# Performance work log

Measured on AMD Instinct MI355X. Metric: run time of the kernel, lower is better.

Reference implementation:

```python
import jax, jax.numpy as jnp
import numpy as np

N_NODES, N_EDGES, DIM, N_LAYERS, N_GRAPHS, N_CLASSES = 50000, 640000, 128, 5, 512, 128


def setup_inputs() -> dict:
    key = jax.random.key(0)
    ks = jax.random.split(key, 10)
    x = jnp.zeros((N_NODES,), dtype=jnp.int32)  # Embedding(1, D) -> all indices 0
    edge_index = jax.random.randint(ks[0], (2, N_EDGES), 0, N_NODES, dtype=jnp.int32)
    edge_attr = jax.random.normal(ks[1], (N_EDGES, DIM), dtype=jnp.float32)
    batch = jnp.sort(jax.random.randint(ks[2], (N_NODES,), 0, N_GRAPHS, dtype=jnp.int32))
    s = 1.0 / np.sqrt(DIM)
    node_emb = jax.random.normal(ks[3], (1, DIM), dtype=jnp.float32)
    Ws = jax.random.normal(ks[4], (N_LAYERS, DIM, DIM), dtype=jnp.float32) * s
    bs = jnp.zeros((N_LAYERS, DIM), dtype=jnp.float32)
    Wes = jax.random.normal(ks[5], (N_LAYERS, DIM, DIM), dtype=jnp.float32) * s
    Wp = jax.random.normal(ks[6], (DIM, N_CLASSES), dtype=jnp.float32) * s
    bp = jnp.zeros((N_CLASSES,), dtype=jnp.float32)
    return {"x": x, "edge_index": edge_index, "edge_attr": edge_attr, "batch": batch,
            "node_emb": node_emb, "Ws": Ws, "bs": bs, "Wes": Wes, "Wp": Wp, "bp": bp}


def reference(x, edge_index, edge_attr, batch, node_emb, Ws, bs, Wes, Wp, bp):
    src, dst = edge_index[0], edge_index[1]
    h = node_emb[x]  # [N, D] embedding lookup (vocab=1)
    n = h.shape[0]
    e = src.shape[0]
    deg = jax.ops.segment_sum(jnp.ones((e,), h.dtype), dst, num_segments=n)
    deg = jnp.maximum(deg, 1.0)[:, None]  # mean aggregation denominator
    for l in range(N_LAYERS):
        hw = h @ Ws[l] + bs[l]                       # [N, D]
        msg = hw[src] + edge_attr @ Wes[l]           # [E, D] gather + edge transform
        agg = jax.ops.segment_sum(msg, dst, num_segments=n) / deg  # scatter-mean
        h = agg + hw                                 # root connection
        if l < N_LAYERS - 1:
            h = jax.nn.relu(h)                       # relu on all but last layer
        # dropout is identity in eval mode
    g = N_GRAPHS
    cnt = jnp.maximum(jax.ops.segment_sum(jnp.ones((n,), h.dtype), batch, num_segments=g), 1.0)
    pooled = jax.ops.segment_sum(h, batch, num_segments=g) / cnt[:, None]  # global_mean_pool
    return pooled @ Wp + bp  # [G, num_clases]
```

## Files before the change

### kernel.cpp

```cpp
#include <hip/hip_runtime.h>

#define N_NODES   50000
#define N_EDGES   640000
#define DIM       128
#define N_LAYERS  5
#define N_GRAPHS  512
#define N_CLASSES 128
#define NB_SCAN   196

typedef __attribute__((ext_vector_type(8))) short short8;
typedef __attribute__((ext_vector_type(4))) float floatx4;

__device__ inline float bfhi(unsigned u) { return __uint_as_float(u & 0xffff0000u); }
__device__ inline float bflo(unsigned u) { return __uint_as_float(u << 16); }
__device__ inline unsigned f2bf(float f) {
  unsigned x = __float_as_uint(f);
  return (x + 0x7fffu + ((x >> 16) & 1u)) >> 16;
}

__global__ void k_zero(int* __restrict__ deg, int* __restrict__ fill,
                       float* __restrict__ pool, float* __restrict__ cnt) {
  int i = blockIdx.x * 256 + threadIdx.x;
  if (i < N_NODES) { deg[i] = 0; fill[i] = 0; }
  if (i < N_GRAPHS * DIM) pool[i] = 0.f;
  if (i < N_GRAPHS) cnt[i] = 0.f;
}

__global__ void k_deg(const int* __restrict__ dst, int* __restrict__ deg) {
  int e = blockIdx.x * 256 + threadIdx.x;
  if (e < N_EDGES) atomicAdd(&deg[dst[e]], 1);
}

__global__ void k_scan1(const int* __restrict__ deg, int* __restrict__ bsum) {
  __shared__ int s[256];
  int t = threadIdx.x, i = blockIdx.x * 256 + t;
  s[t] = (i < N_NODES) ? deg[i] : 0;
  __syncthreads();
  for (int o = 128; o > 0; o >>= 1) {
    if (t < o) s[t] += s[t + o];
    __syncthreads();
  }
  if (t == 0) bsum[blockIdx.x] = s[0];
}

__global__ void k_scan2(int* __restrict__ bsum) {
  __shared__ int s[256];
  int t = threadIdx.x;
  s[t] = (t < NB_SCAN) ? bsum[t] : 0;
  __syncthreads();
  for (int o = 1; o < 256; o <<= 1) {
    int add = (t >= o) ? s[t - o] : 0;
    __syncthreads();
    s[t] += add;
    __syncthreads();
  }
  int ex = (t == 0) ? 0 : s[t - 1];
  if (t < NB_SCAN) bsum[t] = ex;
}

__global__ void k_scan3(const int* __restrict__ deg, const int* __restrict__ bsum,
                        int* __restrict__ row_ptr) {
  __shared__ int s[256];
  int t = threadIdx.x, i = blockIdx.x * 256 + t;
  s[t] = (i < N_NODES) ? deg[i] : 0;
  __syncthreads();
  for (int o = 1; o < 256; o <<= 1) {
    int add = (t >= o) ? s[t - o] : 0;
    __syncthreads();
    s[t] += add;
    __syncthreads();
  }
  int ex = bsum[blockIdx.x] + ((t == 0) ? 0 : s[t - 1]);
  if (i < N_NODES) row_ptr[i] = ex;
  if (blockIdx.x == 0 && t == 0) row_ptr[N_NODES] = N_EDGES;
}

__global__ void k_fill(const int* __restrict__ src, const int* __restrict__ dst,
                       const int* __restrict__ row_ptr, int* __restrict__ fill,
                       int* __restrict__ col_src, int* __restrict__ col_eid) {
  int e = blockIdx.x * 256 + threadIdx.x;
  if (e < N_EDGES) {
    int d = dst[e];
    int pos = row_ptr[d] + atomicAdd(&fill[d], 1);
    col_src[pos] = src[e];
    col_eid[pos] = e;
  }
}

__global__ void k_wconv(const float* __restrict__ Ws, const float* __restrict__ Wes,
                        unsigned short* __restrict__ Wt_s, unsigned short* __restrict__ Wt_e) {
  int idx = blockIdx.x * 256 + threadIdx.x;
  int which = idx / (N_LAYERS * DIM * DIM);
  int rem = idx - which * (N_LAYERS * DIM * DIM);
  int l = rem >> 14;
  int c = (rem >> 7) & 127;
  int k = rem & 127;
  const float* W = which ? Wes : Ws;
  unsigned short* O = which ? Wt_e : Wt_s;
  float v = W[((size_t)l * DIM + k) * DIM + c];
  O[((size_t)l * DIM + c) * DIM + k] = (unsigned short)f2bf(v);
}

__global__ void k_ean_init(const int* __restrict__ row_ptr, const int* __restrict__ col_eid,
                           const float* __restrict__ edge_attr, const int* __restrict__ x,
                           const float* __restrict__ node_emb,
                           unsigned short* __restrict__ ean, float* __restrict__ rdeg,
                           unsigned short* __restrict__ h) {
  int sub = threadIdx.x >> 5;
  int lane = threadIdx.x & 31;
  int i = blockIdx.x * 8 + sub;
  if (i >= N_NODES) return;
  int b = row_ptr[i], e = row_ptr[i + 1];
  float4 acc = make_float4(0.f, 0.f, 0.f, 0.f);
  for (int p = b; p < e; p++) {
    int eid = col_eid[p];
    float4 v = ((const float4*)(edge_attr + (size_t)eid * DIM))[lane];
    acc.x += v.x; acc.y += v.y; acc.z += v.z; acc.w += v.w;
  }
  float r = 1.0f / (float)max(e - b, 1);
  if (lane == 0) rdeg[i] = r;
  uint2 o;
  o.x = f2bf(acc.x * r) | (f2bf(acc.y * r) << 16);
  o.y = f2bf(acc.z * r) | (f2bf(acc.w * r) << 16);
  ((uint2*)(ean + (size_t)i * DIM))[lane] = o;
  float4 hv = ((const float4*)(node_emb + (size_t)x[i] * DIM))[lane];
  uint2 ho;
  ho.x = f2bf(hv.x) | (f2bf(hv.y) << 16);
  ho.y = f2bf(hv.z) | (f2bf(hv.w) << 16);
  ((uint2*)(h + (size_t)i * DIM))[lane] = ho;
}

__global__ void k_gather(const int* __restrict__ row_ptr, const int* __restrict__ col_src,
                         const unsigned short* __restrict__ h, const float* __restrict__ rdeg,
                         unsigned short* __restrict__ u) {
  int sub = threadIdx.x >> 4;
  int lane = threadIdx.x & 15;
  int i = blockIdx.x * 16 + sub;
  if (i >= N_NODES) return;
  int b = row_ptr[i], e = row_ptr[i + 1];
  float a0 = 0.f, a1 = 0.f, a2 = 0.f, a3 = 0.f, a4 = 0.f, a5 = 0.f, a6 = 0.f, a7 = 0.f;
  for (int p = b; p < e; p++) {
    int j = col_src[p];
    uint4 v = *(const uint4*)(h + (size_t)j * DIM + lane * 8);
    a0 += bflo(v.x); a1 += bfhi(v.x);
    a2 += bflo(v.y); a3 += bfhi(v.y);
    a4 += bflo(v.z); a5 += bfhi(v.z);
    a6 += bflo(v.w); a7 += bfhi(v.w);
  }
  float r = rdeg[i];
  uint4 hv = *(const uint4*)(h + (size_t)i * DIM + lane * 8);
  uint4 o;
  o.x = f2bf(bflo(hv.x) + a0 * r) | (f2bf(bfhi(hv.x) + a1 * r) << 16);
  o.y = f2bf(bflo(hv.y) + a2 * r) | (f2bf(bfhi(hv.y) + a3 * r) << 16);
  o.z = f2bf(bflo(hv.z) + a4 * r) | (f2bf(bfhi(hv.z) + a5 * r) << 16);
  o.w = f2bf(bflo(hv.w) + a6 * r) | (f2bf(bfhi(hv.w) + a7 * r) << 16);
  *(uint4*)(u + (size_t)i * DIM + lane * 8) = o;
}

__global__ __launch_bounds__(256) void k_gemm(
    const unsigned short* __restrict__ A0, const unsigned short* __restrict__ A1,
    const unsigned short* __restrict__ W0, const unsigned short* __restrict__ W1,
    const float* __restrict__ bias, unsigned short* __restrict__ hout, int relu) {
  __shared__ unsigned short sA[64][72];
  __shared__ unsigned short sW[128][72];
  int tid = threadIdx.x;
  int wave = tid >> 6, lane = tid & 63;
  int quad = lane >> 4, l16 = lane & 15;
  int row0 = blockIdx.x * 64;
  floatx4 acc[8];
  #pragma unroll
  for (int ci = 0; ci < 8; ci++) acc[ci] = (floatx4){0.f, 0.f, 0.f, 0.f};

  for (int m = 0; m < 2; m++) {
    const unsigned short* A = m ? A1 : A0;
    const unsigned short* W = m ? W1 : W0;
    for (int kc = 0; kc < 128; kc += 64) {
      __syncthreads();
      #pragma unroll
      for (int q = 0; q < 2; q++) {
        int s = tid + 256 * q;
        int r = s >> 3, seg = s & 7;
        int grow = row0 + r;
        uint4 v = make_uint4(0u, 0u, 0u, 0u);
        if (grow < N_NODES)
          v = *(const uint4*)(A + (size_t)grow * DIM + kc + seg * 8);
        *(uint4*)(&sA[r][seg * 8]) = v;
      }
      #pragma unroll
      for (int q = 0; q < 4; q++) {
        int s = tid + 256 * q;
        int r = s >> 3, seg = s & 7;
        *(uint4*)(&sW[r][seg * 8]) =
            *(const uint4*)(W + (size_t)r * DIM + kc + seg * 8);
      }
      __syncthreads();
      #pragma unroll
      for (int ks = 0; ks < 64; ks += 32) {
        short8 a = *(const short8*)(&sA[wave * 16 + l16][ks + quad * 8]);
        #pragma unroll
        for (int ci = 0; ci < 8; ci++) {
          short8 b = *(const short8*)(&sW[ci * 16 + l16][ks + quad * 8]);
          acc[ci] = __builtin_amdgcn_mfma_f32_16x16x32_bf16(a, b, acc[ci], 0, 0, 0);
        }
      }
    }
  }
  #pragma unroll
  for (int ci = 0; ci < 8; ci++) {
    int col = ci * 16 + l16;
    float bv = bias[col];
    #pragma unroll
    for (int r = 0; r < 4; r++) {
      int row = row0 + wave * 16 + quad * 4 + r;
      if (row < N_NODES) {
        float v = acc[ci][r] + bv;
        if (relu) v = fmaxf(v, 0.f);
        hout[(size_t)row * DIM + col] = (unsigned short)f2bf(v);
      }
    }
  }
}

__global__ void k_pool(const unsigned short* __restrict__ h, const int* __restrict__ batch,
                       float* __restrict__ pool, float* __restrict__ cnt) {
  int t = threadIdx.x;
  int i0 = blockIdx.x * 128;
  int iend = min(i0 + 128, N_NODES);
  float acc = 0.f;
  int cur = -1, run = 0;
  for (int i = i0; i < iend; i++) {
    int g = batch[i];
    if (g != cur) {
      if (cur >= 0) {
        atomicAdd(&pool[(size_t)cur * DIM + t], acc);
        if (t == 0) atomicAdd(&cnt[cur], (float)run);
      }
      acc = 0.f; run = 0; cur = g;
    }
    acc += __uint_as_float(((unsigned)h[(size_t)i * DIM + t]) << 16);
    run++;
  }
  if (cur >= 0) {
    atomicAdd(&pool[(size_t)cur * DIM + t], acc);
    if (t == 0) atomicAdd(&cnt[cur], (float)run);
  }
}

__global__ void k_out(const float* __restrict__ pool, const float* __restrict__ cnt,
                      const float* __restrict__ Wp, const float* __restrict__ bp,
                      float* __restrict__ out) {
  __shared__ float sp[DIM];
  int g = blockIdx.x, t = threadIdx.x;
  sp[t] = pool[(size_t)g * DIM + t];
  __syncthreads();
  float r = 1.0f / fmaxf(cnt[g], 1.0f);
  float acc = 0.f;
  for (int k = 0; k < DIM; k++) acc += sp[k] * Wp[(size_t)k * N_CLASSES + t];
  out[(size_t)g * N_CLASSES + t] = acc * r + bp[t];
}

extern "C" void kernel_launch(void* const* d_in, const int* in_sizes, int n_in,
                              void* d_out, int out_size, void* d_ws, size_t ws_size,
                              hipStream_t stream) {
  (void)in_sizes; (void)n_in; (void)out_size; (void)ws_size;
  const int*   x          = (const int*)d_in[0];
  const int*   edge_index = (const int*)d_in[1];
  const float* edge_attr  = (const float*)d_in[2];
  const int*   batch      = (const int*)d_in[3];
  const float* node_emb   = (const float*)d_in[4];
  const float* Ws         = (const float*)d_in[5];
  const float* bs         = (const float*)d_in[6];
  const float* Wes        = (const float*)d_in[7];
  const float* Wp         = (const float*)d_in[8];
  const float* bp         = (const float*)d_in[9];
  float* out = (float*)d_out;
  const int* src = edge_index;
  const int* dst = edge_index + N_EDGES;

  char* p = (char*)d_ws;
  auto alloc = [&](size_t bytes) {
    void* q = (void*)p;
    p += (bytes + 255) & ~(size_t)255;
    return q;
  };
  unsigned short* h    = (unsigned short*)alloc((size_t)N_NODES * DIM * 2);
  unsigned short* u    = (unsigned short*)alloc((size_t)N_NODES * DIM * 2);
  unsigned short* ean  = (unsigned short*)alloc((size_t)N_NODES * DIM * 2);
  unsigned short* Wt_s = (unsigned short*)alloc((size_t)N_LAYERS * DIM * DIM * 2);
  unsigned short* Wt_e = (unsigned short*)alloc((size_t)N_LAYERS * DIM * DIM * 2);
  int*   deg     = (int*)  alloc((size_t)N_NODES * 4);
  float* rdeg    = (float*)alloc((size_t)N_NODES * 4);
  int*   row_ptr = (int*)  alloc((size_t)(N_NODES + 64) * 4);
  int*   fill    = (int*)  alloc((size_t)N_NODES * 4);
  int*   col_src = (int*)  alloc((size_t)N_EDGES * 4);
  int*   col_eid = (int*)  alloc((size_t)N_EDGES * 4);
  float* pool    = (float*)alloc((size_t)N_GRAPHS * DIM * 4);
  float* cnt     = (float*)alloc((size_t)N_GRAPHS * 4);
  int*   bsum    = (int*)  alloc(256 * 4);

  k_zero<<<256, 256, 0, stream>>>(deg, fill, pool, cnt);
  k_deg<<<(N_EDGES + 255) / 256, 256, 0, stream>>>(dst, deg);
  k_scan1<<<NB_SCAN, 256, 0, stream>>>(deg, bsum);
  k_scan2<<<1, 256, 0, stream>>>(bsum);
  k_scan3<<<NB_SCAN, 256, 0, stream>>>(deg, bsum, row_ptr);
  k_fill<<<(N_EDGES + 255) / 256, 256, 0, stream>>>(src, dst, row_ptr, fill, col_src, col_eid);
  k_wconv<<<(2 * N_LAYERS * DIM * DIM) / 256, 256, 0, stream>>>(Ws, Wes, Wt_s, Wt_e);
  k_ean_init<<<(N_NODES + 7) / 8, 256, 0, stream>>>(row_ptr, col_eid, edge_attr, x,
                                                    node_emb, ean, rdeg, h);
  for (int l = 0; l < N_LAYERS; l++) {
    k_gather<<<(N_NODES + 15) / 16, 256, 0, stream>>>(row_ptr, col_src, h, rdeg, u);
    k_gemm<<<(N_NODES + 63) / 64, 256, 0, stream>>>(
        u, ean, Wt_s + (size_t)l * DIM * DIM, Wt_e + (size_t)l * DIM * DIM,
        bs + (size_t)l * DIM, h, (l < N_LAYERS - 1) ? 1 : 0);
  }
  k_pool<<<(N_NODES + 127) / 128, 128, 0, stream>>>(h, batch, pool, cnt);
  k_out<<<N_GRAPHS, N_CLASSES, 0, stream>>>(pool, cnt, Wp, bp, out);
}
```

Baseline: 869.3 us.

## Fuse neighbor gather into layer GEMM with ping-pong node buffers

Merges the per-layer gather kernel into the GEMM kernel. Each block first aggregates neighbor features for its 64 rows directly into shared memory, then runs the MFMA GEMM, which removes the intermediate u buffer round trip and one launch per layer. Because the fused kernel reads h from other nodes while writing output, h is now double-buffered. It also interleaves col_src/col_eid into an int2 array and unrolls the gather loops by two with split accumulators for more memory-level parallelism. The cost is a larger shared-memory footprint (which may reduce occupancy) and a gather phase that sits serially before the GEMM within each block.

```diff
diff --git a/kernel.cpp b/kernel.cpp
--- a/kernel.cpp
+++ b/kernel.cpp
@@ -77,13 +77,12 @@
 
 __global__ void k_fill(const int* __restrict__ src, const int* __restrict__ dst,
                        const int* __restrict__ row_ptr, int* __restrict__ fill,
-                       int* __restrict__ col_src, int* __restrict__ col_eid) {
+                       int2* __restrict__ col) {
   int e = blockIdx.x * 256 + threadIdx.x;
   if (e < N_EDGES) {
     int d = dst[e];
     int pos = row_ptr[d] + atomicAdd(&fill[d], 1);
-    col_src[pos] = src[e];
-    col_eid[pos] = e;
+    col[pos] = make_int2(src[e], e);
   }
 }
 
@@ -101,7 +100,7 @@
   O[((size_t)l * DIM + c) * DIM + k] = (unsigned short)f2bf(v);
 }
 
-__global__ void k_ean_init(const int* __restrict__ row_ptr, const int* __restrict__ col_eid,
+__global__ void k_ean_init(const int* __restrict__ row_ptr, const int2* __restrict__ col,
                            const float* __restrict__ edge_attr, const int* __restrict__ x,
                            const float* __restrict__ node_emb,
                            unsigned short* __restrict__ ean, float* __restrict__ rdeg,
@@ -111,17 +110,27 @@
   int i = blockIdx.x * 8 + sub;
   if (i >= N_NODES) return;
   int b = row_ptr[i], e = row_ptr[i + 1];
-  float4 acc = make_float4(0.f, 0.f, 0.f, 0.f);
-  for (int p = b; p < e; p++) {
-    int eid = col_eid[p];
-    float4 v = ((const float4*)(edge_attr + (size_t)eid * DIM))[lane];
-    acc.x += v.x; acc.y += v.y; acc.z += v.z; acc.w += v.w;
-  }
+  float4 acc0 = make_float4(0.f, 0.f, 0.f, 0.f);
+  float4 acc1 = make_float4(0.f, 0.f, 0.f, 0.f);
+  int p = b;
+  for (; p + 1 < e; p += 2) {
+    int e0 = col[p].y, e1 = col[p + 1].y;
+    float4 v0 = ((const float4*)(edge_attr + (size_t)e0 * DIM))[lane];
+    float4 v1 = ((const float4*)(edge_attr + (size_t)e1 * DIM))[lane];
+    acc0.x += v0.x; acc0.y += v0.y; acc0.z += v0.z; acc0.w += v0.w;
+    acc1.x += v1.x; acc1.y += v1.y; acc1.z += v1.z; acc1.w += v1.w;
+  }
+  if (p < e) {
+    int e0 = col[p].y;
+    float4 v0 = ((const float4*)(edge_attr + (size_t)e0 * DIM))[lane];
+    acc0.x += v0.x; acc0.y += v0.y; acc0.z += v0.z; acc0.w += v0.w;
+  }
+  acc0.x += acc1.x; acc0.y += acc1.y; acc0.z += acc1.z; acc0.w += acc1.w;
   float r = 1.0f / (float)max(e - b, 1);
   if (lane == 0) rdeg[i] = r;
   uint2 o;
-  o.x = f2bf(acc.x * r) | (f2bf(acc.y * r) << 16);
-  o.y = f2bf(acc.z * r) | (f2bf(acc.w * r) << 16);
+  o.x = f2bf(acc0.x * r) | (f2bf(acc0.y * r) << 16);
+  o.y = f2bf(acc0.z * r) | (f2bf(acc0.w * r) << 16);
   ((uint2*)(ean + (size_t)i * DIM))[lane] = o;
   float4 hv = ((const float4*)(node_emb + (size_t)x[i] * DIM))[lane];
   uint2 ho;
@@ -130,62 +139,81 @@
   ((uint2*)(h + (size_t)i * DIM))[lane] = ho;
 }
 
-__global__ void k_gather(const int* __restrict__ row_ptr, const int* __restrict__ col_src,
-                         const unsigned short* __restrict__ h, const float* __restrict__ rdeg,
-                         unsigned short* __restrict__ u) {
-  int sub = threadIdx.x >> 4;
-  int lane = threadIdx.x & 15;
-  int i = blockIdx.x * 16 + sub;
-  if (i >= N_NODES) return;
-  int b = row_ptr[i], e = row_ptr[i + 1];
-  float a0 = 0.f, a1 = 0.f, a2 = 0.f, a3 = 0.f, a4 = 0.f, a5 = 0.f, a6 = 0.f, a7 = 0.f;
-  for (int p = b; p < e; p++) {
-    int j = col_src[p];
-    uint4 v = *(const uint4*)(h + (size_t)j * DIM + lane * 8);
-    a0 += bflo(v.x); a1 += bfhi(v.x);
-    a2 += bflo(v.y); a3 += bfhi(v.y);
-    a4 += bflo(v.z); a5 += bfhi(v.z);
-    a6 += bflo(v.w); a7 += bfhi(v.w);
-  }
-  float r = rdeg[i];
-  uint4 hv = *(const uint4*)(h + (size_t)i * DIM + lane * 8);
-  uint4 o;
-  o.x = f2bf(bflo(hv.x) + a0 * r) | (f2bf(bfhi(hv.x) + a1 * r) << 16);
-  o.y = f2bf(bflo(hv.y) + a2 * r) | (f2bf(bfhi(hv.y) + a3 * r) << 16);
-  o.z = f2bf(bflo(hv.z) + a4 * r) | (f2bf(bfhi(hv.z) + a5 * r) << 16);
-  o.w = f2bf(bflo(hv.w) + a6 * r) | (f2bf(bfhi(hv.w) + a7 * r) << 16);
-  *(uint4*)(u + (size_t)i * DIM + lane * 8) = o;
-}
-
-__global__ __launch_bounds__(256) void k_gemm(
-    const unsigned short* __restrict__ A0, const unsigned short* __restrict__ A1,
+__global__ __launch_bounds__(256) void k_layer(
+    const int* __restrict__ row_ptr, const int2* __restrict__ col,
+    const unsigned short* __restrict__ h, const float* __restrict__ rdeg,
+    const unsigned short* __restrict__ ean,
     const unsigned short* __restrict__ W0, const unsigned short* __restrict__ W1,
     const float* __restrict__ bias, unsigned short* __restrict__ hout, int relu) {
-  __shared__ unsigned short sA[64][72];
+  __shared__ unsigned short sA[64][136];
+  __shared__ unsigned short sE[64][136];
   __shared__ unsigned short sW[128][72];
   int tid = threadIdx.x;
+  int row0 = blockIdx.x * 64;
+
+  #pragma unroll
+  for (int q = 0; q < 4; q++) {
+    int s = tid + 256 * q;
+    int r = s >> 4, seg = s & 15;
+    int grow = row0 + r;
+    uint4 v = make_uint4(0u, 0u, 0u, 0u);
+    if (grow < N_NODES) v = *(const uint4*)(ean + (size_t)grow * DIM + seg * 8);
+    *(uint4*)(&sE[r][seg * 8]) = v;
+  }
+  {
+    int sub = tid >> 4;
+    int lane = tid & 15;
+    for (int n = sub; n < 64; n += 16) {
+      int i = row0 + n;
+      uint4 o = make_uint4(0u, 0u, 0u, 0u);
+      if (i < N_NODES) {
+        int b = row_ptr[i], e = row_ptr[i + 1];
+        float a0 = 0.f, a1 = 0.f, a2 = 0.f, a3 = 0.f;
+        float a4 = 0.f, a5 = 0.f, a6 = 0.f, a7 = 0.f;
+        float b0 = 0.f, b1 = 0.f, b2 = 0.f, b3 = 0.f;
+        float b4 = 0.f, b5 = 0.f, b6 = 0.f, b7 = 0.f;
+        int p = b;
+        for (; p + 1 < e; p += 2) {
+          int j0 = col[p].x, j1 = col[p + 1].x;
+          uint4 v0 = *(const uint4*)(h + (size_t)j0 * DIM + lane * 8);
+          uint4 v1 = *(const uint4*)(h + (size_t)j1 * DIM + lane * 8);
+          a0 += bflo(v0.x); a1 += bfhi(v0.x); a2 += bflo(v0.y); a3 += bfhi(v0.y);
+          a4 += bflo(v0.z); a5 += bfhi(v0.z); a6 += bflo(v0.w); a7 += bfhi(v0.w);
+          b0 += bflo(v1.x); b1 += bfhi(v1.x); b2 += bflo(v1.y); b3 += bfhi(v1.y);
+          b4 += bflo(v1.z); b5 += bfhi(v1.z); b6 += bflo(v1.w); b7 += bfhi(v1.w);
+        }
+        if (p < e) {
+          int j0 = col[p].x;
+          uint4 v0 = *(const uint4*)(h + (size_t)j0 * DIM + lane * 8);
+          a0 += bflo(v0.x); a1 += bfhi(v0.x); a2 += bflo(v0.y); a3 += bfhi(v0.y);
+          a4 += bflo(v0.z); a5 += bfhi(v0.z); a6 += bflo(v0.w); a7 += bfhi(v0.w);
+        }
+        a0 += b0; a1 += b1; a2 += b2; a3 += b3;
+        a4 += b4; a5 += b5; a6 += b6; a7 += b7;
+        float r = rdeg[i];
+        uint4 hv = *(const uint4*)(h + (size_t)i * DIM + lane * 8);
+        o.x = f2bf(bflo(hv.x) + a0 * r) | (f2bf(bfhi(hv.x) + a1 * r) << 16);
+        o.y = f2bf(bflo(hv.y) + a2 * r) | (f2bf(bfhi(hv.y) + a3 * r) << 16);
+        o.z = f2bf(bflo(hv.z) + a4 * r) | (f2bf(bfhi(hv.z) + a5 * r) << 16);
+        o.w = f2bf(bflo(hv.w) + a6 * r) | (f2bf(bfhi(hv.w) + a7 * r) << 16);
+      }
+      *(uint4*)(&sA[n][lane * 8]) = o;
+    }
+  }
+  __syncthreads();
+
   int wave = tid >> 6, lane = tid & 63;
   int quad = lane >> 4, l16 = lane & 15;
-  int row0 = blockIdx.x * 64;
   floatx4 acc[8];
   #pragma unroll
   for (int ci = 0; ci < 8; ci++) acc[ci] = (floatx4){0.f, 0.f, 0.f, 0.f};
 
+  #pragma unroll
   for (int m = 0; m < 2; m++) {
-    const unsigned short* A = m ? A1 : A0;
     const unsigned short* W = m ? W1 : W0;
+    #pragma unroll
     for (int kc = 0; kc < 128; kc += 64) {
-      __syncthreads();
-      #pragma unroll
-      for (int q = 0; q < 2; q++) {
-        int s = tid + 256 * q;
-        int r = s >> 3, seg = s & 7;
-        int grow = row0 + r;
-        uint4 v = make_uint4(0u, 0u, 0u, 0u);
-        if (grow < N_NODES)
-          v = *(const uint4*)(A + (size_t)grow * DIM + kc + seg * 8);
-        *(uint4*)(&sA[r][seg * 8]) = v;
-      }
+      if (m | kc) __syncthreads();
       #pragma unroll
       for (int q = 0; q < 4; q++) {
         int s = tid + 256 * q;
@@ -196,7 +224,8 @@
       __syncthreads();
       #pragma unroll
       for (int ks = 0; ks < 64; ks += 32) {
-        short8 a = *(const short8*)(&sA[wave * 16 + l16][ks + quad * 8]);
+        short8 a = m ? *(const short8*)(&sE[wave * 16 + l16][kc + ks + quad * 8])
+                     : *(const short8*)(&sA[wave * 16 + l16][kc + ks + quad * 8]);
         #pragma unroll
         for (int ci = 0; ci < 8; ci++) {
           short8 b = *(const short8*)(&sW[ci * 16 + l16][ks + quad * 8]);
@@ -207,15 +236,15 @@
   }
   #pragma unroll
   for (int ci = 0; ci < 8; ci++) {
-    int col = ci * 16 + l16;
-    float bv = bias[col];
+    int c = ci * 16 + l16;
+    float bv = bias[c];
     #pragma unroll
     for (int r = 0; r < 4; r++) {
       int row = row0 + wave * 16 + quad * 4 + r;
       if (row < N_NODES) {
         float v = acc[ci][r] + bv;
         if (relu) v = fmaxf(v, 0.f);
-        hout[(size_t)row * DIM + col] = (unsigned short)f2bf(v);
+        hout[(size_t)row * DIM + c] = (unsigned short)f2bf(v);
       }
     }
   }
@@ -284,7 +313,7 @@
     return q;
   };
   unsigned short* h    = (unsigned short*)alloc((size_t)N_NODES * DIM * 2);
-  unsigned short* u    = (unsigned short*)alloc((size_t)N_NODES * DIM * 2);
+  unsigned short* hb   = (unsigned short*)alloc((size_t)N_NODES * DIM * 2);
   unsigned short* ean  = (unsigned short*)alloc((size_t)N_NODES * DIM * 2);
   unsigned short* Wt_s = (unsigned short*)alloc((size_t)N_LAYERS * DIM * DIM * 2);
   unsigned short* Wt_e = (unsigned short*)alloc((size_t)N_LAYERS * DIM * DIM * 2);
@@ -292,8 +321,7 @@
   float* rdeg    = (float*)alloc((size_t)N_NODES * 4);
   int*   row_ptr = (int*)  alloc((size_t)(N_NODES + 64) * 4);
   int*   fill    = (int*)  alloc((size_t)N_NODES * 4);
-  int*   col_src = (int*)  alloc((size_t)N_EDGES * 4);
-  int*   col_eid = (int*)  alloc((size_t)N_EDGES * 4);
+  int2*  col     = (int2*) alloc((size_t)N_EDGES * 8);
   float* pool    = (float*)alloc((size_t)N_GRAPHS * DIM * 4);
   float* cnt     = (float*)alloc((size_t)N_GRAPHS * 4);
   int*   bsum    = (int*)  alloc(256 * 4);
@@ -303,16 +331,19 @@
   k_scan1<<<NB_SCAN, 256, 0, stream>>>(deg, bsum);
   k_scan2<<<1, 256, 0, stream>>>(bsum);
   k_scan3<<<NB_SCAN, 256, 0, stream>>>(deg, bsum, row_ptr);
-  k_fill<<<(N_EDGES + 255) / 256, 256, 0, stream>>>(src, dst, row_ptr, fill, col_src, col_eid);
+  k_fill<<<(N_EDGES + 255) / 256, 256, 0, stream>>>(src, dst, row_ptr, fill, col);
   k_wconv<<<(2 * N_LAYERS * DIM * DIM) / 256, 256, 0, stream>>>(Ws, Wes, Wt_s, Wt_e);
-  k_ean_init<<<(N_NODES + 7) / 8, 256, 0, stream>>>(row_ptr, col_eid, edge_attr, x,
+  k_ean_init<<<(N_NODES + 7) / 8, 256, 0, stream>>>(row_ptr, col, edge_attr, x,
                                                     node_emb, ean, rdeg, h);
+  unsigned short* cur = h;
+  unsigned short* nxt = hb;
   for (int l = 0; l < N_LAYERS; l++) {
-    k_gather<<<(N_NODES + 15) / 16, 256, 0, stream>>>(row_ptr, col_src, h, rdeg, u);
-    k_gemm<<<(N_NODES + 63) / 64, 256, 0, stream>>>(
-        u, ean, Wt_s + (size_t)l * DIM * DIM, Wt_e + (size_t)l * DIM * DIM,
-        bs + (size_t)l * DIM, h, (l < N_LAYERS - 1) ? 1 : 0);
-  }
-  k_pool<<<(N_NODES + 127) / 128, 128, 0, stream>>>(h, batch, pool, cnt);
+    k_layer<<<(N_NODES + 63) / 64, 256, 0, stream>>>(
+        row_ptr, col, cur, rdeg, ean,
+        Wt_s + (size_t)l * DIM * DIM, Wt_e + (size_t)l * DIM * DIM,
+        bs + (size_t)l * DIM, nxt, (l < N_LAYERS - 1) ? 1 : 0);
+    unsigned short* t = cur; cur = nxt; nxt = t;
+  }
+  k_pool<<<(N_NODES + 127) / 128, 128, 0, stream>>>(cur, batch, pool, cnt);
   k_out<<<N_GRAPHS, N_CLASSES, 0, stream>>>(pool, cnt, Wp, bp, out);
 }
```

New measurement: 948.9 us. +9.1%, slower.
